# Kernel tuning notes

Hardware: AMD Instinct MI355X
Metric: run time of the kernel (lower is better)

Reference implementation:

```python
import jax, jax.numpy as jnp
import numpy as np

WIN = (16, 9, 9)
WIN_SIZE = WIN[0] * WIN[1] * WIN[2]  # 1296
EPS = float(np.e ** -15)             # ~3.06e-7, matches np.power(np.e, -15)


def setup_inputs() -> dict:
    key = jax.random.key(0)
    k1, k2 = jax.random.split(key)
    shape = (2, 1, 96, 192, 192)  # [B, 1, D, H, W]
    I = jax.random.normal(k1, shape, dtype=jnp.float32)
    J = jax.random.normal(k2, shape, dtype=jnp.float32)
    return {"I": I, "J": J}


def _box_sums(tmp):
    # Grouped conv3d with an all-ones [5,1,16,9,9] kernel: per-channel sliding
    k = jnp.ones((5, 1) + WIN, dtype=tmp.dtype)
    return jax.lax.conv_general_dilated(
        tmp, k,
        window_strides=(1, 1, 1),
        padding=[(0, 0), (WIN[1] // 2, WIN[1] // 2), (WIN[2] // 2, WIN[2] // 2)],
        feature_group_count=5,
        dimension_numbers=("NCDHW", "OIDHW", "NCDHW"),
    )


def reference(I, J):
    # I, J: [B, 1, D, H, W]
    tmp = jnp.concatenate([I, J, I * I, J * J, I * J], axis=1)  # [B,5,D,H,W]
    sums = _box_sums(tmp)  # [B, 5, D-15, H, W]
    I_sum, J_sum = sums[:, 0], sums[:, 1]
    I2_sum, J2_sum, IJ_sum = sums[:, 2], sums[:, 3], sums[:, 4]

    u_I = I_sum / WIN_SIZE
    u_J = J_sum / WIN_SIZE

    cross = IJ_sum - u_J * I_sum - u_I * J_sum + u_I * u_J * WIN_SIZE
    I_var = I2_sum - 2.0 * u_I * I_sum + u_I * u_I * WIN_SIZE
    J_var = J2_sum - 2.0 * u_J * J_sum + u_J * u_J * WIN_SIZE

    nz = (I_var * J_var) > EPS  # bool_non_zero; where false, substitute 1.0
    cross = jnp.where(nz, cross, 1.0)
    I_var = jnp.where(nz, I_var, 1.0)
    J_var = jnp.where(nz, J_var, 1.0)

    cc = cross * cross / (I_var * J_var + EPS)  # [B, D-15, H, W]
    loss = -1.0 * jnp.mean(cc, axis=(1, 2, 3)) + 1.0  # [B]
    return loss, cc
```

## Files before the change

### kernel.cpp

```cpp
#include <hip/hip_runtime.h>


constexpr int N = 2, D = 96, H = 192, W = 192;
constexpr int OD = 81;
constexpr int KD = 16;
constexpr int HWp = H * W;
constexpr float INV_WIN = 1.0f / 1296.0f;
constexpr float EPS_NZ = 3.0590232050182579e-07f;
constexpr int CH = 24;
constexpr int ODPB = 14;

__device__ __forceinline__ unsigned bf16rne(float f) {
  unsigned u = __float_as_uint(f);
  return (u + 0x7fffu + ((u >> 16) & 1u)) >> 16;
}
__device__ __forceinline__ float bf16tof(unsigned h) {
  return __uint_as_float(h << 16);
}

__global__ __launch_bounds__(192)
void k_dw(const float* __restrict__ I, const float* __restrict__ J,
          unsigned* __restrict__ ws, int od0, int c, int odcStride) {
  const int h = blockIdx.x;
  const int n = blockIdx.z;
  const int os = od0 + blockIdx.y * ODPB;
  int oe = od0 + c; if (os + ODPB < oe) oe = os + ODPB;
  if (os >= oe) return;
  const int w = threadIdx.x;

  __shared__ float4 x4[2][W + 8];
  __shared__ float  x1[2][W + 8];
  __shared__ float4 a4[2][W + 8];
  __shared__ float  a1[2][W + 8];

  if (w < 4) {
    x4[0][w] = make_float4(0.f,0.f,0.f,0.f); x1[0][w] = 0.f;
    x4[1][w] = make_float4(0.f,0.f,0.f,0.f); x1[1][w] = 0.f;
  }
  if (w >= W - 4) {
    x4[0][w + 8] = make_float4(0.f,0.f,0.f,0.f); x1[0][w + 8] = 0.f;
    x4[1][w + 8] = make_float4(0.f,0.f,0.f,0.f); x1[1][w + 8] = 0.f;
  }
  __syncthreads();

  const size_t colBase = ((size_t)n * D * H + h) * (size_t)W + w;
  const float* Ip = I + colBase;
  const float* Jp = J + colBase;
  unsigned* wbase = ws + ((size_t)n * odcStride * HWp + (size_t)h * W + w) * 3;

  int pe = -1;
  if (w < 3) pe = w + 1;
  else if (w >= W - 3) pe = w + 7;
  const int p = 4 + w;

  float sI = 0.f, sJ = 0.f, sII = 0.f, sJJ = 0.f, sIJ = 0.f;
  for (int d = os; d < os + KD - 1; ++d) {
    const float iv = Ip[(size_t)d * HWp];
    const float jv = Jp[(size_t)d * HWp];
    sI += iv; sJ += jv;
    sII += iv * iv; sJJ += jv * jv; sIJ += iv * jv;
  }

  int od = os;
  float eI0 = Ip[(size_t)(od + KD - 1) * HWp];
  float eJ0 = Jp[(size_t)(od + KD - 1) * HWp];
  float lI0 = Ip[(size_t)od * HWp];
  float lJ0 = Jp[(size_t)od * HWp];
  float eI1 = 0.f, eJ1 = 0.f, lI1 = 0.f, lJ1 = 0.f;
  if (od + 1 < oe) {
    eI1 = Ip[(size_t)(od + KD) * HWp];
    eJ1 = Jp[(size_t)(od + KD) * HWp];
    lI1 = Ip[(size_t)(od + 1) * HWp];
    lJ1 = Jp[(size_t)(od + 1) * HWp];
  }

  while (od < oe) {
    const bool two = (od + 1 < oe);
    const float ceI0 = eI0, ceJ0 = eJ0, clI0 = lI0, clJ0 = lJ0;
    const float ceI1 = eI1, ceJ1 = eJ1, clI1 = lI1, clJ1 = lJ1;
    const int odn = od + 2;
    if (odn < oe) {
      eI0 = Ip[(size_t)(odn + KD - 1) * HWp];
      eJ0 = Jp[(size_t)(odn + KD - 1) * HWp];
      lI0 = Ip[(size_t)odn * HWp];
      lJ0 = Jp[(size_t)odn * HWp];
      if (odn + 1 < oe) {
        eI1 = Ip[(size_t)(odn + KD) * HWp];
        eJ1 = Jp[(size_t)(odn + KD) * HWp];
        lI1 = Ip[(size_t)(odn + 1) * HWp];
        lJ1 = Jp[(size_t)(odn + 1) * HWp];
      }
    }
    sI += ceI0; sJ += ceJ0;
    sII += ceI0 * ceI0; sJJ += ceJ0 * ceJ0; sIJ += ceI0 * ceJ0;
    x4[0][p] = make_float4(sI, sJ, sII, sJJ); x1[0][p] = sIJ;
    sI -= clI0; sJ -= clJ0;
    sII -= clI0 * clI0; sJJ -= clJ0 * clJ0; sIJ -= clI0 * clJ0;
    if (two) {
      sI += ceI1; sJ += ceJ1;
      sII += ceI1 * ceI1; sJJ += ceJ1 * ceJ1; sIJ += ceI1 * ceJ1;
      x4[1][p] = make_float4(sI, sJ, sII, sJJ); x1[1][p] = sIJ;
      sI -= clI1; sJ -= clJ1;
      sII -= clI1 * clI1; sJJ -= clJ1 * clJ1; sIJ -= clI1 * clJ1;
    }
    asm volatile("s_waitcnt lgkmcnt(0)" ::: "memory");
    __builtin_amdgcn_s_barrier();
    {
      float4 m0 = x4[0][p - 1], m1 = x4[0][p], m2 = x4[0][p + 1];
      a4[0][p] = make_float4(m0.x + m1.x + m2.x, m0.y + m1.y + m2.y,
                             m0.z + m1.z + m2.z, m0.w + m1.w + m2.w);
      a1[0][p] = x1[0][p - 1] + x1[0][p] + x1[0][p + 1];
      if (pe >= 0) {
        float4 e0 = x4[0][pe - 1], e1 = x4[0][pe], e2 = x4[0][pe + 1];
        a4[0][pe] = make_float4(e0.x + e1.x + e2.x, e0.y + e1.y + e2.y,
                                e0.z + e1.z + e2.z, e0.w + e1.w + e2.w);
        a1[0][pe] = x1[0][pe - 1] + x1[0][pe] + x1[0][pe + 1];
      }
    }
    if (two) {
      float4 m0 = x4[1][p - 1], m1 = x4[1][p], m2 = x4[1][p + 1];
      a4[1][p] = make_float4(m0.x + m1.x + m2.x, m0.y + m1.y + m2.y,
                             m0.z + m1.z + m2.z, m0.w + m1.w + m2.w);
      a1[1][p] = x1[1][p - 1] + x1[1][p] + x1[1][p + 1];
      if (pe >= 0) {
        float4 e0 = x4[1][pe - 1], e1 = x4[1][pe], e2 = x4[1][pe + 1];
        a4[1][pe] = make_float4(e0.x + e1.x + e2.x, e0.y + e1.y + e2.y,
                                e0.z + e1.z + e2.z, e0.w + e1.w + e2.w);
        a1[1][pe] = x1[1][pe - 1] + x1[1][pe] + x1[1][pe + 1];
      }
    }
    asm volatile("s_waitcnt lgkmcnt(0)" ::: "memory");
    __builtin_amdgcn_s_barrier();
    {
      float4 b0 = a4[0][p - 3], b1 = a4[0][p], b2 = a4[0][p + 3];
      const float r0 = b0.x + b1.x + b2.x;
      const float r1 = b0.y + b1.y + b2.y;
      const float r2 = b0.z + b1.z + b2.z;
      const float r3 = b0.w + b1.w + b2.w;
      const float r4 = a1[0][p - 3] + a1[0][p] + a1[0][p + 3];
      unsigned* o = wbase + (size_t)(od - od0) * HWp * 3;
      *(uint3*)o = make_uint3(bf16rne(r0) | (bf16rne(r1) << 16),
                              bf16rne(r2) | (bf16rne(r3) << 16),
                              bf16rne(r4));
    }
    if (two) {
      float4 b0 = a4[1][p - 3], b1 = a4[1][p], b2 = a4[1][p + 3];
      const float r0 = b0.x + b1.x + b2.x;
      const float r1 = b0.y + b1.y + b2.y;
      const float r2 = b0.z + b1.z + b2.z;
      const float r3 = b0.w + b1.w + b2.w;
      const float r4 = a1[1][p - 3] + a1[1][p] + a1[1][p + 3];
      unsigned* o = wbase + (size_t)(od + 1 - od0) * HWp * 3;
      *(uint3*)o = make_uint3(bf16rne(r0) | (bf16rne(r1) << 16),
                              bf16rne(r2) | (bf16rne(r3) << 16),
                              bf16rne(r4));
    }
    od += 2;
  }
}

__global__ __launch_bounds__(192)
void k_hcc(const unsigned* __restrict__ ws, float* __restrict__ cc,
           float* __restrict__ acc, int od0, int odcStride) {
  const int odi = blockIdx.x;
  const int od = od0 + odi;
  const int h0 = blockIdx.y * CH;
  const int n = blockIdx.z;
  const int w = threadIdx.x;
  const unsigned* base =
      ws + ((size_t)n * odcStride * HWp + (size_t)odi * HWp + w) * 3;
  float* ccp = cc + ((size_t)n * OD + od) * (size_t)HWp + w;

  float s0 = 0.f, s1 = 0.f, s2 = 0.f, s3 = 0.f, s4 = 0.f;
  float lsum = 0.f;
  uint3 hist[8];
  const uint3 z3 = make_uint3(0u, 0u, 0u);

  uint3 vN = z3;
  {
    const int hin = h0 - 4;
    if (hin >= 0) vN = *(const uint3*)(base + (size_t)hin * W * 3);
  }
#pragma unroll
  for (int t = 0; t < CH + 8; ++t) {
    const uint3 v = vN;
    if (t + 1 < CH + 8) {
      const int hn = h0 - 4 + t + 1;
      vN = (hn >= 0 && hn < H) ? *(const uint3*)(base + (size_t)hn * W * 3) : z3;
    }
    s0 += bf16tof(v.x & 0xffffu); s1 += bf16tof(v.x >> 16);
    s2 += bf16tof(v.y & 0xffffu); s3 += bf16tof(v.y >> 16);
    s4 += bf16tof(v.z & 0xffffu);
    if (t >= 8) {
      const int h = h0 + t - 8;
      const float cross = s4 - s0 * s1 * INV_WIN;
      const float vI = s2 - s0 * s0 * INV_WIN;
      const float vJ = s3 - s1 * s1 * INV_WIN;
      const float prod = vI * vJ;
      const float c = (prod > EPS_NZ) ? (cross * cross) / (prod + EPS_NZ)
                                      : 1.0f / (1.0f + EPS_NZ);
      ccp[(size_t)h * W] = c;
      lsum += c;
      const uint3 q = hist[t & 7];
      s0 -= bf16tof(q.x & 0xffffu); s1 -= bf16tof(q.x >> 16);
      s2 -= bf16tof(q.y & 0xffffu); s3 -= bf16tof(q.y >> 16);
      s4 -= bf16tof(q.z & 0xffffu);
    }
    hist[t & 7] = v;
  }
  __shared__ float red[3];
#pragma unroll
  for (int off = 32; off > 0; off >>= 1) lsum += __shfl_xor(lsum, off, 64);
  if ((threadIdx.x & 63) == 0) red[threadIdx.x >> 6] = lsum;
  __syncthreads();
  if (threadIdx.x == 0) atomicAdd(acc + n, red[0] + red[1] + red[2]);
}

__global__ void k_fin(const float* __restrict__ acc, float* __restrict__ out) {
  if (threadIdx.x < N)
    out[threadIdx.x] = 1.0f - acc[threadIdx.x] * (1.0f / 2985984.0f);
}

extern "C" void kernel_launch(void* const* d_in, const int* in_sizes, int n_in,
                              void* d_out, int out_size, void* d_ws,
                              size_t ws_size, hipStream_t stream) {
  const float* I = (const float*)d_in[0];
  const float* J = (const float*)d_in[1];
  float* out = (float*)d_out;
  float* acc = (float*)d_ws;
  unsigned* planes = (unsigned*)((char*)d_ws + 256);

  hipMemsetAsync(d_ws, 0, 2 * sizeof(float), stream);

  const size_t perOdPerN = (size_t)HWp * 12;
  size_t avail = (ws_size > 256) ? (ws_size - 256) : 0;
  long long odcMax = (long long)(avail / (2 * perOdPerN));
  if (odcMax < 1) odcMax = 1;
  if (odcMax > OD) odcMax = OD;
  const int odc = (int)odcMax;

  float* ccOut = out + 2;
  for (int od0 = 0; od0 < OD; od0 += odc) {
    const int c = (odc < OD - od0) ? odc : (OD - od0);
    const int S = (c + ODPB - 1) / ODPB;
    hipLaunchKernelGGL(k_dw, dim3(H, S, N), dim3(192), 0, stream,
                       I, J, planes, od0, c, odc);
    hipLaunchKernelGGL(k_hcc, dim3(c, H / CH, N), dim3(192), 0, stream,
                       planes, ccOut, acc, od0, odc);
  }
  hipLaunchKernelGGL(k_fin, dim3(1), dim3(64), 0, stream, acc, out);
}
```

Measured before the change: 72.53 us.

## Split bf16 workspace into three planar arrays and halve H chunk size

Changes the intermediate workspace from an interleaved uint3-per-pixel layout to three separate planes (one per packed word), so writes and reads become unit-stride dword accesses across threads instead of 12-byte strided vector accesses. It also halves the H chunk per block in the second kernel, which doubles the block count and adds more halo re-reads of the 8-row window. The plane stride assumes the workspace holds 2*odcStride*HWp entries per plane.

```diff
diff --git a/kernel.cpp b/kernel.cpp
--- a/kernel.cpp
+++ b/kernel.cpp
@@ -7,7 +7,7 @@
 constexpr int HWp = H * W;
 constexpr float INV_WIN = 1.0f / 1296.0f;
 constexpr float EPS_NZ = 3.0590232050182579e-07f;
-constexpr int CH = 24;
+constexpr int CH = 12;
 constexpr int ODPB = 14;
 
 __device__ __forceinline__ unsigned bf16rne(float f) {
@@ -46,7 +46,10 @@
   const size_t colBase = ((size_t)n * D * H + h) * (size_t)W + w;
   const float* Ip = I + colBase;
   const float* Jp = J + colBase;
-  unsigned* wbase = ws + ((size_t)n * odcStride * HWp + (size_t)h * W + w) * 3;
+  const size_t PS = (size_t)2 * odcStride * HWp;
+  unsigned* wp0 = ws + ((size_t)n * odcStride) * HWp + (size_t)h * W + w;
+  unsigned* wp1 = wp0 + PS;
+  unsigned* wp2 = wp0 + 2 * PS;
 
   int pe = -1;
   if (w < 3) pe = w + 1;
@@ -138,10 +141,10 @@
       const float r2 = b0.z + b1.z + b2.z;
       const float r3 = b0.w + b1.w + b2.w;
       const float r4 = a1[0][p - 3] + a1[0][p] + a1[0][p + 3];
-      unsigned* o = wbase + (size_t)(od - od0) * HWp * 3;
-      *(uint3*)o = make_uint3(bf16rne(r0) | (bf16rne(r1) << 16),
-                              bf16rne(r2) | (bf16rne(r3) << 16),
-                              bf16rne(r4));
+      const size_t idx = (size_t)(od - od0) * HWp;
+      wp0[idx] = bf16rne(r0) | (bf16rne(r1) << 16);
+      wp1[idx] = bf16rne(r2) | (bf16rne(r3) << 16);
+      wp2[idx] = bf16rne(r4);
     }
     if (two) {
       float4 b0 = a4[1][p - 3], b1 = a4[1][p], b2 = a4[1][p + 3];
@@ -150,10 +153,10 @@
       const float r2 = b0.z + b1.z + b2.z;
       const float r3 = b0.w + b1.w + b2.w;
       const float r4 = a1[1][p - 3] + a1[1][p] + a1[1][p + 3];
-      unsigned* o = wbase + (size_t)(od + 1 - od0) * HWp * 3;
-      *(uint3*)o = make_uint3(bf16rne(r0) | (bf16rne(r1) << 16),
-                              bf16rne(r2) | (bf16rne(r3) << 16),
-                              bf16rne(r4));
+      const size_t idx = (size_t)(od + 1 - od0) * HWp;
+      wp0[idx] = bf16rne(r0) | (bf16rne(r1) << 16);
+      wp1[idx] = bf16rne(r2) | (bf16rne(r3) << 16);
+      wp2[idx] = bf16rne(r4);
     }
     od += 2;
   }
@@ -167,30 +170,38 @@
   const int h0 = blockIdx.y * CH;
   const int n = blockIdx.z;
   const int w = threadIdx.x;
-  const unsigned* base =
-      ws + ((size_t)n * odcStride * HWp + (size_t)odi * HWp + w) * 3;
+  const size_t PS = (size_t)2 * odcStride * HWp;
+  const unsigned* b0 =
+      ws + ((size_t)n * odcStride + odi) * HWp + w;
+  const unsigned* b1 = b0 + PS;
+  const unsigned* b2 = b0 + 2 * PS;
   float* ccp = cc + ((size_t)n * OD + od) * (size_t)HWp + w;
 
   float s0 = 0.f, s1 = 0.f, s2 = 0.f, s3 = 0.f, s4 = 0.f;
   float lsum = 0.f;
-  uint3 hist[8];
-  const uint3 z3 = make_uint3(0u, 0u, 0u);
-
-  uint3 vN = z3;
+  unsigned h0r[8], h1r[8], h2r[8];
+
+  unsigned v0 = 0u, v1 = 0u, v2 = 0u;
   {
     const int hin = h0 - 4;
-    if (hin >= 0) vN = *(const uint3*)(base + (size_t)hin * W * 3);
+    if (hin >= 0) {
+      const size_t off = (size_t)hin * W;
+      v0 = b0[off]; v1 = b1[off]; v2 = b2[off];
+    }
   }
 #pragma unroll
   for (int t = 0; t < CH + 8; ++t) {
-    const uint3 v = vN;
+    const unsigned c0 = v0, c1 = v1, c2 = v2;
     if (t + 1 < CH + 8) {
       const int hn = h0 - 4 + t + 1;
-      vN = (hn >= 0 && hn < H) ? *(const uint3*)(base + (size_t)hn * W * 3) : z3;
-    }
-    s0 += bf16tof(v.x & 0xffffu); s1 += bf16tof(v.x >> 16);
-    s2 += bf16tof(v.y & 0xffffu); s3 += bf16tof(v.y >> 16);
-    s4 += bf16tof(v.z & 0xffffu);
+      if (hn >= 0 && hn < H) {
+        const size_t off = (size_t)hn * W;
+        v0 = b0[off]; v1 = b1[off]; v2 = b2[off];
+      } else { v0 = 0u; v1 = 0u; v2 = 0u; }
+    }
+    s0 += bf16tof(c0 & 0xffffu); s1 += bf16tof(c0 >> 16);
+    s2 += bf16tof(c1 & 0xffffu); s3 += bf16tof(c1 >> 16);
+    s4 += bf16tof(c2 & 0xffffu);
     if (t >= 8) {
       const int h = h0 + t - 8;
       const float cross = s4 - s0 * s1 * INV_WIN;
@@ -201,12 +212,12 @@
                                       : 1.0f / (1.0f + EPS_NZ);
       ccp[(size_t)h * W] = c;
       lsum += c;
-      const uint3 q = hist[t & 7];
-      s0 -= bf16tof(q.x & 0xffffu); s1 -= bf16tof(q.x >> 16);
-      s2 -= bf16tof(q.y & 0xffffu); s3 -= bf16tof(q.y >> 16);
-      s4 -= bf16tof(q.z & 0xffffu);
-    }
-    hist[t & 7] = v;
+      const unsigned q0 = h0r[t & 7], q1 = h1r[t & 7], q2 = h2r[t & 7];
+      s0 -= bf16tof(q0 & 0xffffu); s1 -= bf16tof(q0 >> 16);
+      s2 -= bf16tof(q1 & 0xffffu); s3 -= bf16tof(q1 >> 16);
+      s4 -= bf16tof(q2 & 0xffffu);
+    }
+    h0r[t & 7] = c0; h1r[t & 7] = c1; h2r[t & 7] = c2;
   }
   __shared__ float red[3];
 #pragma unroll
```

New measurement: 90.85 us. +25.2%, slower.
